# Performance work log

Measured on AMD Instinct MI355X. Metric: run time of the kernel, lower is better.

The kernel has to match this reference:

```python
import jax, jax.numpy as jnp
import numpy as np

N_HEADS = 1
D_MODEL = 128
TOP_K = 64
BATCH = 4
SEQ = 4096


def _rope_tables(T, d_head):
    # div_term = 10000**(arange(0,d,2)/d), repeat_interleave(2); even slice recovers the base freqs
    pos = jnp.arange(T, dtype=jnp.float32)[:, None]            # (T,1)
    div = 10000.0 ** (jnp.arange(0, d_head, 2, dtype=jnp.float32) / d_head)  # (d/2,)
    ang = pos / div[None, :]                                    # (T, d/2)
    return jnp.cos(ang), jnp.sin(ang)


def _apply_rope(x, cos, sin):
    # x: (..., T, d); cos/sin: (T, d/2) broadcast over leading dims
    xe = x[..., 0::2]
    xo = x[..., 1::2]
    re = xe * cos - xo * sin
    ro = xe * sin + xo * cos
    return jnp.stack([re, ro], axis=-1).reshape(x.shape)


def setup_inputs() -> dict:
    key = jax.random.key(0)
    kq, kk, kv = jax.random.split(key, 3)
    q = jax.random.normal(kq, (BATCH, SEQ, D_MODEL), dtype=jnp.float32)
    k = jax.random.normal(kk, (BATCH, SEQ, D_MODEL), dtype=jnp.float32)
    v = jax.random.normal(kv, (BATCH, SEQ, D_MODEL), dtype=jnp.float32)
    return {"q": q, "k": k, "v": v}


def reference(q, k, v):
    b, T, d_model = q.shape
    H = N_HEADS
    D = d_model // H  # d_head; module only valid for H=1 (k is never head-split)
    qh = q.reshape(b, T, H, D).transpose(0, 2, 1, 3)   # (b,H,T,D)
    vh = v.reshape(b, T, H, D).transpose(0, 2, 1, 3)   # (b,H,T,D)
    kh = k[:, None, :, :]                              # (b,1,T,d_model) == (b,H,T,D) for H=1

    cos, sin = _rope_tables(T, D)
    qh = _apply_rope(qh, cos, sin)
    kh = _apply_rope(kh, cos, sin)

    scale = 1.0 / jnp.sqrt(jnp.asarray(D, dtype=qh.dtype))
    logits = jnp.einsum('bhtd,bhsd->bhts', qh, kh) * scale   # (b,H,T,T)

    idx = jnp.arange(T)
    causal = idx[None, :] <= idx[:, None]                    # (T,T): key j <= query i
    logits = jnp.where(causal[None, None], logits, -jnp.inf)

    topk_vals, topk_idx = jax.lax.top_k(logits, TOP_K)       # (b,H,T,K)
    attn = jax.nn.softmax(topk_vals, axis=-1)                # -inf rows -> 0 weight

    bi = jnp.arange(b)[:, None, None, None]
    hi = jnp.arange(H)[None, :, None, None]
    topk_v = vh[bi, hi, topk_idx]                            # (b,H,T,K,D)
    out = jnp.einsum('bhtk,bhtkd->bhtd', attn, topk_v)       # (b,H,T,D)
    return out.transpose(0, 2, 1, 3).reshape(b, T, d_model)
```

## Files before the change

kernel.cpp:

```cpp
#include <hip/hip_runtime.h>
#include <math.h>

#define BATCH 4
#define SEQ   4096
#define DM    128
#define TOPK  64
#define SCALE 0.08838834764831845f
#define CAP   384

typedef short bf16x8 __attribute__((ext_vector_type(8)));
typedef float f32x4  __attribute__((ext_vector_type(4)));

__device__ __forceinline__ unsigned short f2bf(float x) {
    unsigned u = __float_as_uint(x);
    u += 0x7FFFu + ((u >> 16) & 1u);
    return (unsigned short)(u >> 16);
}
__device__ __forceinline__ float bf2f(unsigned short h) {
    return __uint_as_float(((unsigned)h) << 16);
}
__device__ __forceinline__ void split3(float x, unsigned short& h,
                                       unsigned short& md, unsigned short& l) {
    h = f2bf(x);
    float r1 = x - bf2f(h);
    md = f2bf(r1);
    float r2 = r1 - bf2f(md);
    l = f2bf(r2);
}

__device__ __forceinline__ unsigned fmap(float f) {
    unsigned u = __float_as_uint(f);
    return (u & 0x80000000u) ? ~u : (u | 0x80000000u);
}
__device__ __forceinline__ float finv(unsigned u) {
    return (u & 0x80000000u) ? __uint_as_float(u & 0x7FFFFFFFu) : __uint_as_float(~u);
}
__device__ __forceinline__ float wave_fmax(float v) {
    #pragma unroll
    for (int m = 32; m; m >>= 1) v = fmaxf(v, __shfl_xor(v, m));
    return v;
}
__device__ __forceinline__ float wave_fsum(float v) {
    #pragma unroll
    for (int m = 32; m; m >>= 1) v += __shfl_xor(v, m);
    return v;
}
__device__ __forceinline__ int wave_isum(int v) {
    #pragma unroll
    for (int m = 32; m; m >>= 1) v += __shfl_xor(v, m);
    return v;
}
__device__ __forceinline__ unsigned wave_umax(unsigned v) {
    #pragma unroll
    for (int m = 32; m; m >>= 1) { unsigned o = __shfl_xor(v, m); v = (o > v) ? o : v; }
    return v;
}

__global__ void rope_decomp(const float* __restrict__ q, const float* __restrict__ k,
                            unsigned short* __restrict__ qh, unsigned short* __restrict__ qm,
                            unsigned short* __restrict__ ql, unsigned short* __restrict__ kh,
                            unsigned short* __restrict__ km, unsigned short* __restrict__ kl) {
    int idx = blockIdx.x * blockDim.x + threadIdx.x;
    const int total = BATCH * SEQ * (DM / 2);
    if (idx >= total) return;
    int i   = idx & 63;
    int pos = (idx >> 6) & (SEQ - 1);
    int b   = idx >> 18;
    float dv  = powf(10000.0f, (float)(2 * i) / (float)DM);
    float ang = (float)pos / dv;
    float sn, cs;
    sincosf(ang, &sn, &cs);
    size_t base = ((size_t)b * SEQ + pos) * DM + 2 * i;
    float qe = q[base], qo = q[base + 1];
    float ke = k[base], ko = k[base + 1];
    float q0 = (qe * cs - qo * sn) * SCALE, q1 = (qe * sn + qo * cs) * SCALE;
    float k0 = ke * cs - ko * sn,          k1 = ke * sn + ko * cs;
    unsigned short h, m2, l;
    split3(q0, h, m2, l); qh[base] = h;     qm[base] = m2;     ql[base] = l;
    split3(q1, h, m2, l); qh[base + 1] = h; qm[base + 1] = m2; ql[base + 1] = l;
    split3(k0, h, m2, l); kh[base] = h;     km[base] = m2;     kl[base] = l;
    split3(k1, h, m2, l); kh[base + 1] = h; km[base + 1] = m2; kl[base + 1] = l;
}

__launch_bounds__(256, 2)
__global__ void logits_mfma(const unsigned short* __restrict__ qh, const unsigned short* __restrict__ qm,
                            const unsigned short* __restrict__ ql, const unsigned short* __restrict__ kh,
                            const unsigned short* __restrict__ km, const unsigned short* __restrict__ kl,
                            float* __restrict__ lg, int r0, int m, int stride) {
    const int st = blockIdx.x, qt = blockIdx.y, b = blockIdx.z;
    const int Q0 = r0 + qt * 128, S0 = st * 128;
    if (S0 > Q0 + 127) return;
    const int tid = threadIdx.x, lane = tid & 63, w = tid >> 6;
    const int wm = (w >> 1) * 64, wn = (w & 1) * 64;
    if (S0 + wn > Q0 + wm + 63) return;

    const int rA = Q0 + wm + (lane & 15);
    const int rB = S0 + wn + (lane & 15);
    const int dc = (lane >> 4) * 8;

    f32x4 acc[4][4] = {};
    #pragma unroll
    for (int kk = 0; kk < 4; ++kk) {
        const int doff = kk * 32 + dc;
        bf16x8 Ah[4], Am[4], Al[4], Bh[4], Bm[4], Bl[4];
        #pragma unroll
        for (int i = 0; i < 4; ++i) {
            size_t qoff = ((size_t)b * SEQ + rA + i * 16) * DM + doff;
            Ah[i] = *(const bf16x8*)(qh + qoff);
            Am[i] = *(const bf16x8*)(qm + qoff);
            Al[i] = *(const bf16x8*)(ql + qoff);
            size_t koff = ((size_t)b * SEQ + rB + i * 16) * DM + doff;
            Bh[i] = *(const bf16x8*)(kh + koff);
            Bm[i] = *(const bf16x8*)(km + koff);
            Bl[i] = *(const bf16x8*)(kl + koff);
        }
        #pragma unroll
        for (int i = 0; i < 4; ++i)
            #pragma unroll
            for (int j = 0; j < 4; ++j) {
                f32x4 c = acc[i][j];
                c = __builtin_amdgcn_mfma_f32_16x16x32_bf16(Ah[i], Bh[j], c, 0, 0, 0);
                c = __builtin_amdgcn_mfma_f32_16x16x32_bf16(Ah[i], Bm[j], c, 0, 0, 0);
                c = __builtin_amdgcn_mfma_f32_16x16x32_bf16(Am[i], Bh[j], c, 0, 0, 0);
                c = __builtin_amdgcn_mfma_f32_16x16x32_bf16(Ah[i], Bl[j], c, 0, 0, 0);
                c = __builtin_amdgcn_mfma_f32_16x16x32_bf16(Al[i], Bh[j], c, 0, 0, 0);
                c = __builtin_amdgcn_mfma_f32_16x16x32_bf16(Am[i], Bm[j], c, 0, 0, 0);
                acc[i][j] = c;
            }
    }

    const int colb = lane & 15, rowb = (lane >> 4) * 4;
    #pragma unroll
    for (int i = 0; i < 4; ++i) {
        #pragma unroll
        for (int r = 0; r < 4; ++r) {
            int qrow = Q0 + wm + i * 16 + rowb + r;
            size_t base = ((size_t)(b * m + (qrow - r0))) * stride;
            #pragma unroll
            for (int j = 0; j < 4; ++j) {
                int col = S0 + wn + j * 16 + colb;
                if (col <= qrow) lg[base + col] = acc[i][j][r];
            }
        }
    }
}

__launch_bounds__(256)
__global__ void select_out2(const float* __restrict__ lg, const float* __restrict__ v,
                            float* __restrict__ out, int r0, int m, int stride) {
    __shared__ unsigned long long bufK[4][CAP];
    __shared__ float sW[4][TOPK];
    __shared__ int   sI[4][TOPK];
    __shared__ int   cnt[4];

    const int w = threadIdx.x >> 6, lane = threadIdx.x & 63;
    const int x = blockIdx.x * 4 + w, b = blockIdx.y;
    if (x >= m) return;
    const int t = r0 + x, n = t + 1;
    const float* row = lg + ((size_t)(b * m + x)) * stride;
    const float4* row4 = (const float4*)row;
    const int nv4 = n >> 2, rem = n & 3;

    if (n <= TOPK) {
        float val = (lane < n) ? row[lane] : -3.0e38f;
        float M = wave_fmax(val);
        float wgt = (lane < n) ? expf(val - M) : 0.f;
        float S = wave_fsum(wgt);
        sW[w][lane] = wgt;
        float inv = 1.f / S;
        float a0 = 0.f, a1 = 0.f;
        for (int j = 0; j < n; ++j) {
            float wj = sW[w][j];
            size_t base = ((size_t)b * SEQ + j) * DM;
            a0 += wj * v[base + lane];
            a1 += wj * v[base + 64 + lane];
        }
        size_t ob = ((size_t)b * SEQ + t) * DM;
        out[ob + lane] = a0 * inv;
        out[ob + 64 + lane] = a1 * inv;
        return;
    }

    float T;
    if (n <= 300) {
        T = -3.0e38f;
    } else {
        float p  = 128.f / (float)n;
        float tt = sqrtf(-2.f * logf(p));
        T = tt - (2.30753f + 0.27061f * tt) / (1.f + 0.99229f * tt + 0.04481f * tt * tt);
    }

    unsigned um = 0u;
    float Tlo = -3.3e38f, Thi = 3.3e38f;
    int C = 0;
    for (int it = 0; it < 24; ++it) {
        int c = 0;
        unsigned lm = 0u;
        for (int i = lane; i < nv4; i += 64) {
            float4 r4 = row4[i];
            c += (r4.x >= T) + (r4.y >= T) + (r4.z >= T) + (r4.w >= T);
            if (it == 0) {
                unsigned u0 = fmap(r4.x), u1 = fmap(r4.y), u2 = fmap(r4.z), u3 = fmap(r4.w);
                unsigned a = u0 > u1 ? u0 : u1, bb = u2 > u3 ? u2 : u3;
                a = a > bb ? a : bb;
                lm = a > lm ? a : lm;
            }
        }
        if (lane < rem) {
            float val = row[nv4 * 4 + lane];
            c += (val >= T);
            if (it == 0) { unsigned u = fmap(val); lm = u > lm ? u : lm; }
        }
        C = wave_isum(c);
        if (it == 0) um = wave_umax(lm);
        if (C >= TOPK && C <= CAP) break;
        if (C < TOPK) Thi = T; else Tlo = T;
        if (Tlo > -3.2e38f && Thi < 3.2e38f) T = 0.5f * (Tlo + Thi);
        else if (C < TOPK)                   T = T - 0.45f;
        else                                 T = T + 0.35f;
    }
    const float M = finv(um);

    if (lane == 0) cnt[w] = 0;
    for (int i = lane; i < nv4; i += 64) {
        float4 r4 = row4[i];
        int s = i << 2;
        if (r4.x >= T) { int p = atomicAdd(&cnt[w], 1); if (p < CAP) bufK[w][p] = ((unsigned long long)fmap(r4.x) << 32) | (unsigned)(SEQ - s); }
        if (r4.y >= T) { int p = atomicAdd(&cnt[w], 1); if (p < CAP) bufK[w][p] = ((unsigned long long)fmap(r4.y) << 32) | (unsigned)(SEQ - (s + 1)); }
        if (r4.z >= T) { int p = atomicAdd(&cnt[w], 1); if (p < CAP) bufK[w][p] = ((unsigned long long)fmap(r4.z) << 32) | (unsigned)(SEQ - (s + 2)); }
        if (r4.w >= T) { int p = atomicAdd(&cnt[w], 1); if (p < CAP) bufK[w][p] = ((unsigned long long)fmap(r4.w) << 32) | (unsigned)(SEQ - (s + 3)); }
    }
    if (lane < rem) {
        float val = row[nv4 * 4 + lane];
        if (val >= T) { int p = atomicAdd(&cnt[w], 1); if (p < CAP) bufK[w][p] = ((unsigned long long)fmap(val) << 32) | (unsigned)(SEQ - (nv4 * 4 + lane)); }
    }
    int Cw = cnt[w];
    if (Cw > CAP) Cw = CAP;

    for (int c0 = lane; c0 < Cw; c0 += 64) {
        unsigned long long kc = bufK[w][c0];
        int r = 0;
        for (int j = 0; j < Cw; ++j) r += (bufK[w][j] > kc);
        if (r < TOPK) {
            sW[w][r] = expf(finv((unsigned)(kc >> 32)) - M);
            sI[w][r] = SEQ - (int)(kc & 0xFFFFFFFFu);
        }
    }

    float S = wave_fsum(sW[w][lane]);
    float inv = 1.f / S;

    float a0 = 0.f, a1 = 0.f;
    #pragma unroll 4
    for (int j = 0; j < TOPK; ++j) {
        float wj = sW[w][j];
        int idx = sI[w][j];
        size_t base = ((size_t)b * SEQ + idx) * DM;
        a0 += wj * v[base + lane];
        a1 += wj * v[base + 64 + lane];
    }
    size_t ob = ((size_t)b * SEQ + t) * DM;
    out[ob + lane] = a0 * inv;
    out[ob + 64 + lane] = a1 * inv;
}

__global__ void rope_prep(const float* __restrict__ q, const float* __restrict__ k,
                          float* __restrict__ rq, float* __restrict__ rk) {
    int idx = blockIdx.x * blockDim.x + threadIdx.x;
    const int total = BATCH * SEQ * (DM / 2);
    if (idx >= total) return;
    int i   = idx & 63;
    int pos = (idx >> 6) & (SEQ - 1);
    int b   = idx >> 18;
    float dv  = powf(10000.0f, (float)(2 * i) / (float)DM);
    float ang = (float)pos / dv;
    float sn, cs;
    sincosf(ang, &sn, &cs);
    size_t base = ((size_t)b * SEQ + pos) * DM + 2 * i;
    float qe = q[base], qo = q[base + 1];
    float ke = k[base], ko = k[base + 1];
    rq[base]     = qe * cs - qo * sn;
    rq[base + 1] = qe * sn + qo * cs;
    rk[base]     = ke * cs - ko * sn;
    rk[base + 1] = ke * sn + ko * cs;
}

__launch_bounds__(256)
__global__ void topk_attn(const float* __restrict__ rq, const float* __restrict__ rk,
                          const float* __restrict__ v, float* __restrict__ out) {
    __shared__ unsigned umap[SEQ];
    __shared__ float    qs[DM];
    __shared__ int      selIdx[TOPK];
    __shared__ float    selW[TOPK];
    __shared__ int      cnt;
    __shared__ float    redf[4];
    __shared__ int      redi[4];
    __shared__ float    sMax, sSum;

    const int t   = blockIdx.x & (SEQ - 1);
    const int b   = blockIdx.x >> 12;
    const int tid = threadIdx.x;
    const int lane = tid & 63, wid = tid >> 6;
    const int n = t + 1;

    if (tid < DM) qs[tid] = rq[((size_t)b * SEQ + t) * DM + tid];
    if (tid == 0) cnt = 0;
    __syncthreads();

    float lmax = -INFINITY;
    for (int s = tid; s < n; s += 256) {
        const float4* kr = (const float4*)(rk + ((size_t)b * SEQ + s) * DM);
        const float4* qr = (const float4*)qs;
        float acc = 0.f;
        #pragma unroll
        for (int d = 0; d < DM / 4; ++d) {
            float4 kv = kr[d]; float4 qv = qr[d];
            acc += kv.x * qv.x + kv.y * qv.y + kv.z * qv.z + kv.w * qv.w;
        }
        float lgv = acc * SCALE;
        umap[s] = fmap(lgv);
        lmax = fmaxf(lmax, lgv);
    }
    #pragma unroll
    for (int off = 32; off; off >>= 1) lmax = fmaxf(lmax, __shfl_down(lmax, off));
    if (lane == 0) redf[wid] = lmax;
    __syncthreads();
    if (tid == 0) sMax = fmaxf(fmaxf(redf[0], redf[1]), fmaxf(redf[2], redf[3]));
    __syncthreads();
    const float M = sMax;

    const int K = (n < TOPK) ? n : TOPK;
    unsigned thr = 0u;
    if (n > TOPK) {
        unsigned long long lo = 0ull, hi = (unsigned long long)fmap(M);
        while (lo < hi) {
            unsigned long long mid = (lo + hi + 1ull) >> 1;
            unsigned m32 = (unsigned)mid;
            int c = 0;
            for (int s = tid; s < n; s += 256) c += (umap[s] >= m32) ? 1 : 0;
            #pragma unroll
            for (int off = 32; off; off >>= 1) c += __shfl_down(c, off);
            if (lane == 0) redi[wid] = c;
            __syncthreads();
            int tot = redi[0] + redi[1] + redi[2] + redi[3];
            __syncthreads();
            if (tot >= K) lo = mid; else hi = mid - 1ull;
        }
        thr = (unsigned)lo;
    }

    for (int s = tid; s < n; s += 256) {
        if (umap[s] > thr) {
            int p = atomicAdd(&cnt, 1);
            if (p < TOPK) { selIdx[p] = s; selW[p] = expf(finv(umap[s]) - M); }
        }
    }
    __syncthreads();
    for (int s = tid; s < n; s += 256) {
        if (umap[s] == thr) {
            int p = atomicAdd(&cnt, 1);
            if (p < TOPK) { selIdx[p] = s; selW[p] = expf(finv(umap[s]) - M); }
        }
    }
    __syncthreads();
    const int nsel = (cnt < TOPK) ? cnt : TOPK;

    if (tid < 64) {
        float w = (tid < nsel) ? selW[tid] : 0.f;
        #pragma unroll
        for (int off = 32; off; off >>= 1) w += __shfl_down(w, off);
        if (tid == 0) sSum = w;
    }
    __syncthreads();
    const float inv = 1.0f / sSum;

    if (tid < DM) {
        float a = 0.f;
        for (int j = 0; j < nsel; ++j)
            a += selW[j] * v[((size_t)b * SEQ + selIdx[j]) * DM + tid];
        out[((size_t)b * SEQ + t) * DM + tid] = a * inv;
    }
}

extern "C" void kernel_launch(void* const* d_in, const int* in_sizes, int n_in,
                              void* d_out, int out_size, void* d_ws, size_t ws_size,
                              hipStream_t stream) {
    const float* q = (const float*)d_in[0];
    const float* k = (const float*)d_in[1];
    const float* v = (const float*)d_in[2];
    float* out = (float*)d_out;

    const size_t plane = (size_t)BATCH * SEQ * DM;
    const size_t planesBytes = 6 * plane * sizeof(unsigned short);

    long long Wb = (long long)ws_size - (long long)planesBytes;
    int cr0[64], cm[64], nch = 0;
    bool ok = (Wb > 0);
    int r0 = 0;
    while (ok && r0 < SEQ) {
        int m = SEQ - r0;
        while (m >= 128) {
            long long stride = ((r0 + m + 127) / 128) * 128;
            long long bytes = (long long)BATCH * m * stride * 4;
            if (bytes <= Wb) break;
            m -= 128;
        }
        if (m < 128 || nch >= 64) { ok = false; break; }
        cr0[nch] = r0; cm[nch] = m; ++nch;
        r0 += m;
    }

    const int total = BATCH * SEQ * (DM / 2);

    if (!ok) {
        float* rq = (float*)d_ws;
        float* rk = rq + plane;
        hipLaunchKernelGGL(rope_prep, dim3((total + 255) / 256), dim3(256), 0, stream,
                           q, k, rq, rk);
        hipLaunchKernelGGL(topk_attn, dim3(BATCH * SEQ), dim3(256), 0, stream,
                           rq, rk, v, out);
        return;
    }

    unsigned short* qh = (unsigned short*)d_ws;
    unsigned short* qm = qh + plane;
    unsigned short* ql = qm + plane;
    unsigned short* kh = ql + plane;
    unsigned short* km = kh + plane;
    unsigned short* kl = km + plane;
    float* lgbuf = (float*)((char*)d_ws + planesBytes);

    hipLaunchKernelGGL(rope_decomp, dim3((total + 255) / 256), dim3(256), 0, stream,
                       q, k, qh, qm, ql, kh, km, kl);

    for (int c = 0; c < nch; ++c) {
        const int R0 = cr0[c], M = cm[c];
        const int stride = ((R0 + M + 127) / 128) * 128;
        dim3 g1((R0 + M + 127) / 128, M / 128, BATCH);
        hipLaunchKernelGGL(logits_mfma, g1, dim3(256), 0, stream,
                           qh, qm, ql, kh, km, kl, lgbuf, R0, M, stride);
        dim3 g2((M + 3) / 4, BATCH);
        hipLaunchKernelGGL(select_out2, g2, dim3(256), 0, stream,
                           lgbuf, v, out, R0, M, stride);
    }
}
```

Before: 247.0 us.

## Fuse threshold search with candidate collection and vectorize top-k V gather

The per-row top-k threshold search in select_out2 now collects candidates into the shared buffer in the same pass that counts them, which removes the separate final collection pass over the logits row. The next threshold guess comes from a normal-quantile estimate of the observed count (secant-like), with bisection as the fallback, and the iteration cap drops from 24 to 12. The V weighted sum now uses float4 loads with the wave split into two halves over the top-k entries, then combines them with a shuffle. The trade-off is atomics on every search iteration, and a less robust search if the quantile model fits the logit distribution poorly.

```diff
diff --git a/kernel.cpp b/kernel.cpp
--- a/kernel.cpp
+++ b/kernel.cpp
@@ -45,15 +45,17 @@
     for (int m = 32; m; m >>= 1) v += __shfl_xor(v, m);
     return v;
 }
-__device__ __forceinline__ int wave_isum(int v) {
-    #pragma unroll
-    for (int m = 32; m; m >>= 1) v += __shfl_xor(v, m);
-    return v;
-}
 __device__ __forceinline__ unsigned wave_umax(unsigned v) {
     #pragma unroll
     for (int m = 32; m; m >>= 1) { unsigned o = __shfl_xor(v, m); v = (o > v) ? o : v; }
     return v;
+}
+
+__device__ __forceinline__ float ztail(float p) {
+    float pp = (p <= 0.5f) ? p : (1.f - p);
+    float tt = sqrtf(-2.f * logf(pp));
+    float z = tt - (2.30753f + 0.27061f * tt) / (1.f + 0.99229f * tt + 0.04481f * tt * tt);
+    return (p <= 0.5f) ? z : -z;
 }
 
 __global__ void rope_decomp(const float* __restrict__ q, const float* __restrict__ k,
@@ -181,61 +183,49 @@
         return;
     }
 
-    float T;
-    if (n <= 300) {
-        T = -3.0e38f;
-    } else {
-        float p  = 128.f / (float)n;
-        float tt = sqrtf(-2.f * logf(p));
-        T = tt - (2.30753f + 0.27061f * tt) / (1.f + 0.99229f * tt + 0.04481f * tt * tt);
-    }
-
-    unsigned um = 0u;
+    float T, zt = 0.f;
+    if (n <= CAP - 32) T = -3.0e38f;
+    else { zt = ztail(128.f / (float)n); T = zt; }
+
     float Tlo = -3.3e38f, Thi = 3.3e38f;
     int C = 0;
-    for (int it = 0; it < 24; ++it) {
-        int c = 0;
+    unsigned um = 0u;
+    for (int it = 0; it < 12; ++it) {
+        if (lane == 0) cnt[w] = 0;
         unsigned lm = 0u;
         for (int i = lane; i < nv4; i += 64) {
             float4 r4 = row4[i];
-            c += (r4.x >= T) + (r4.y >= T) + (r4.z >= T) + (r4.w >= T);
-            if (it == 0) {
-                unsigned u0 = fmap(r4.x), u1 = fmap(r4.y), u2 = fmap(r4.z), u3 = fmap(r4.w);
-                unsigned a = u0 > u1 ? u0 : u1, bb = u2 > u3 ? u2 : u3;
-                a = a > bb ? a : bb;
-                lm = a > lm ? a : lm;
-            }
+            int s = i << 2;
+            if (r4.x >= T) { unsigned u = fmap(r4.x); lm = u > lm ? u : lm; int p = atomicAdd(&cnt[w], 1); if (p < CAP) bufK[w][p] = ((unsigned long long)u << 32) | (unsigned)(SEQ - s); }
+            if (r4.y >= T) { unsigned u = fmap(r4.y); lm = u > lm ? u : lm; int p = atomicAdd(&cnt[w], 1); if (p < CAP) bufK[w][p] = ((unsigned long long)u << 32) | (unsigned)(SEQ - (s + 1)); }
+            if (r4.z >= T) { unsigned u = fmap(r4.z); lm = u > lm ? u : lm; int p = atomicAdd(&cnt[w], 1); if (p < CAP) bufK[w][p] = ((unsigned long long)u << 32) | (unsigned)(SEQ - (s + 2)); }
+            if (r4.w >= T) { unsigned u = fmap(r4.w); lm = u > lm ? u : lm; int p = atomicAdd(&cnt[w], 1); if (p < CAP) bufK[w][p] = ((unsigned long long)u << 32) | (unsigned)(SEQ - (s + 3)); }
         }
         if (lane < rem) {
             float val = row[nv4 * 4 + lane];
-            c += (val >= T);
-            if (it == 0) { unsigned u = fmap(val); lm = u > lm ? u : lm; }
-        }
-        C = wave_isum(c);
-        if (it == 0) um = wave_umax(lm);
+            if (val >= T) { unsigned u = fmap(val); lm = u > lm ? u : lm; int p = atomicAdd(&cnt[w], 1); if (p < CAP) bufK[w][p] = ((unsigned long long)u << 32) | (unsigned)(SEQ - (nv4 * 4 + lane)); }
+        }
+        um = wave_umax(lm);
+        C = cnt[w];
         if (C >= TOPK && C <= CAP) break;
-        if (C < TOPK) Thi = T; else Tlo = T;
-        if (Tlo > -3.2e38f && Thi < 3.2e38f) T = 0.5f * (Tlo + Thi);
-        else if (C < TOPK)                   T = T - 0.45f;
-        else                                 T = T + 0.35f;
+        if (C < TOPK) Thi = fminf(Thi, T); else Tlo = fmaxf(Tlo, T);
+        float Tn; bool okc = false;
+        float phat = (float)(C < 1 ? 1 : C) / (float)n;
+        if (phat < 0.45f && T > 0.05f) {
+            float zh = ztail(phat);
+            if (zh > 0.05f) { Tn = T * (zt / zh); okc = true; }
+        }
+        if (!okc || !(Tn > Tlo && Tn < Thi)) {
+            if (Tlo > -3.2e38f && Thi < 3.2e38f) Tn = 0.5f * (Tlo + Thi);
+            else if (C < TOPK)                   Tn = T - 0.5f;
+            else                                 Tn = T + 0.4f;
+        }
+        T = Tn;
     }
     const float M = finv(um);
-
-    if (lane == 0) cnt[w] = 0;
-    for (int i = lane; i < nv4; i += 64) {
-        float4 r4 = row4[i];
-        int s = i << 2;
-        if (r4.x >= T) { int p = atomicAdd(&cnt[w], 1); if (p < CAP) bufK[w][p] = ((unsigned long long)fmap(r4.x) << 32) | (unsigned)(SEQ - s); }
-        if (r4.y >= T) { int p = atomicAdd(&cnt[w], 1); if (p < CAP) bufK[w][p] = ((unsigned long long)fmap(r4.y) << 32) | (unsigned)(SEQ - (s + 1)); }
-        if (r4.z >= T) { int p = atomicAdd(&cnt[w], 1); if (p < CAP) bufK[w][p] = ((unsigned long long)fmap(r4.z) << 32) | (unsigned)(SEQ - (s + 2)); }
-        if (r4.w >= T) { int p = atomicAdd(&cnt[w], 1); if (p < CAP) bufK[w][p] = ((unsigned long long)fmap(r4.w) << 32) | (unsigned)(SEQ - (s + 3)); }
-    }
-    if (lane < rem) {
-        float val = row[nv4 * 4 + lane];
-        if (val >= T) { int p = atomicAdd(&cnt[w], 1); if (p < CAP) bufK[w][p] = ((unsigned long long)fmap(val) << 32) | (unsigned)(SEQ - (nv4 * 4 + lane)); }
-    }
-    int Cw = cnt[w];
-    if (Cw > CAP) Cw = CAP;
+    int Cw = C; if (Cw > CAP) Cw = CAP;
+
+    sW[w][lane] = 0.f; sI[w][lane] = 0;
 
     for (int c0 = lane; c0 < Cw; c0 += 64) {
         unsigned long long kc = bufK[w][c0];
@@ -246,22 +236,26 @@
             sI[w][r] = SEQ - (int)(kc & 0xFFFFFFFFu);
         }
     }
-
     float S = wave_fsum(sW[w][lane]);
     float inv = 1.f / S;
 
-    float a0 = 0.f, a1 = 0.f;
-    #pragma unroll 4
-    for (int j = 0; j < TOPK; ++j) {
-        float wj = sW[w][j];
-        int idx = sI[w][j];
-        size_t base = ((size_t)b * SEQ + idx) * DM;
-        a0 += wj * v[base + lane];
-        a1 += wj * v[base + 64 + lane];
-    }
-    size_t ob = ((size_t)b * SEQ + t) * DM;
-    out[ob + lane] = a0 * inv;
-    out[ob + 64 + lane] = a1 * inv;
+    const int sub = lane & 31, halfw = lane >> 5;
+    f32x4 a4 = {0.f, 0.f, 0.f, 0.f};
+    for (int j2 = halfw; j2 < TOPK; j2 += 2) {
+        float wj = sW[w][j2];
+        const float4* vr = (const float4*)(v + ((size_t)b * SEQ + sI[w][j2]) * DM) + sub;
+        float4 vv = *vr;
+        a4.x += wj * vv.x; a4.y += wj * vv.y; a4.z += wj * vv.z; a4.w += wj * vv.w;
+    }
+    a4.x += __shfl_xor(a4.x, 32);
+    a4.y += __shfl_xor(a4.y, 32);
+    a4.z += __shfl_xor(a4.z, 32);
+    a4.w += __shfl_xor(a4.w, 32);
+    if (halfw == 0) {
+        float4 o4;
+        o4.x = a4.x * inv; o4.y = a4.y * inv; o4.z = a4.z * inv; o4.w = a4.w * inv;
+        *((float4*)(out + ((size_t)b * SEQ + t) * DM) + sub) = o4;
+    }
 }
 
 __global__ void rope_prep(const float* __restrict__ q, const float* __restrict__ k,
@@ -391,13 +385,14 @@
     float* out = (float*)d_out;
 
     const size_t plane = (size_t)BATCH * SEQ * DM;
-    const size_t planesBytes = 6 * plane * sizeof(unsigned short);
-
-    long long Wb = (long long)ws_size - (long long)planesBytes;
+    const size_t planesB = 6 * plane * sizeof(unsigned short);
+    const int total = BATCH * SEQ * (DM / 2);
+
+    long long Wb = (long long)ws_size - (long long)planesB;
     int cr0[64], cm[64], nch = 0;
-    bool ok = (Wb > 0);
+    bool okc = (Wb > 0);
     int r0 = 0;
-    while (ok && r0 < SEQ) {
+    while (okc && r0 < SEQ) {
         int m = SEQ - r0;
         while (m >= 128) {
             long long stride = ((r0 + m + 127) / 128) * 128;
@@ -405,14 +400,12 @@
             if (bytes <= Wb) break;
             m -= 128;
         }
-        if (m < 128 || nch >= 64) { ok = false; break; }
+        if (m < 128 || nch >= 64) { okc = false; break; }
         cr0[nch] = r0; cm[nch] = m; ++nch;
         r0 += m;
     }
 
-    const int total = BATCH * SEQ * (DM / 2);
-
-    if (!ok) {
+    if (!okc) {
         float* rq = (float*)d_ws;
         float* rk = rq + plane;
         hipLaunchKernelGGL(rope_prep, dim3((total + 255) / 256), dim3(256), 0, stream,
@@ -428,7 +421,7 @@
     unsigned short* kh = ql + plane;
     unsigned short* km = kh + plane;
     unsigned short* kl = km + plane;
-    float* lgbuf = (float*)((char*)d_ws + planesBytes);
+    float* lgbuf = (float*)((char*)d_ws + planesB);
 
     hipLaunchKernelGGL(rope_decomp, dim3((total + 255) / 256), dim3(256), 0, stream,
                        q, k, qh, qm, ql, kh, km, kl);
```

Result: no change. 242.8 us, median of 2 (-1.7%).
